# Kernel tuning notes

Measured on AMD Instinct MI355X. Metric: run time of the kernel, lower is better.

The kernel has to match this reference:

```python
import jax, jax.numpy as jnp
import numpy as np

B, S, D = 2, 4096, 512   # batch, seq_len, input_dim
W, H = 256, 4            # memory width (d_model), attention heads
DH = W // H              # per-head depth


def _dense(x, w, b):
    return x @ w + b


def setup_inputs() -> dict:
    key = jax.random.key(0)
    ks = jax.random.split(key, 24)
    def w(k, shape):
        return jax.random.normal(k, shape, dtype=jnp.float32) * 0.02
    inp = {
        "x": jax.random.normal(ks[0], (B, S, D), dtype=jnp.float32),
        # outer q/k/v projections D -> W
        "qp_w": w(ks[1], (D, W)), "qp_b": jnp.zeros((W,), jnp.float32),
        "kp_w": w(ks[2], (D, W)), "kp_b": jnp.zeros((W,), jnp.float32),
        "vp_w": w(ks[3], (D, W)), "vp_b": jnp.zeros((W,), jnp.float32),
        # MHA internal projections W -> W
        "wq_w": w(ks[4], (W, W)), "wq_b": jnp.zeros((W,), jnp.float32),
        "wk_w": w(ks[5], (W, W)), "wk_b": jnp.zeros((W,), jnp.float32),
        "wv_w": w(ks[6], (W, W)), "wv_b": jnp.zeros((W,), jnp.float32),
        "wo_w": w(ks[7], (W, W)), "wo_b": jnp.zeros((W,), jnp.float32),
        # deep MLP memory (depth=2, gelu) + its output proj W -> W
        "m0_w": w(ks[8], (W, W)), "m0_b": jnp.zeros((W,), jnp.float32),
        "m1_w": w(ks[9], (W, W)), "m1_b": jnp.zeros((W,), jnp.float32),
        "mo_w": w(ks[10], (W, W)), "mo_b": jnp.zeros((W,), jnp.float32),
        # final output projection W -> D
        "op_w": w(ks[11], (W, D)), "op_b": jnp.zeros((D,), jnp.float32),
    }
    return inp


def reference(x, qp_w, qp_b, kp_w, kp_b, vp_w, vp_b,
              wq_w, wq_b, wk_w, wk_b, wv_w, wv_b, wo_w, wo_b,
              m0_w, m0_b, m1_w, m1_b, mo_w, mo_b, op_w, op_b):
    # outer projections (D -> W)
    q0 = _dense(x, qp_w, qp_b)
    k0 = _dense(x, kp_w, kp_b)
    v0 = _dense(x, vp_w, vp_b)
    # MHA internal projections (W -> W)
    q = _dense(q0, wq_w, wq_b)
    k = _dense(k0, wk_w, wk_b)
    v = _dense(v0, wv_w, wv_b)
    # split heads: [B,S,W] -> [B,H,S,DH]
    def split(t):
        return t.reshape(B, S, H, DH).transpose(0, 2, 1, 3)
    qh, kh, vh = split(q), split(k), split(v)
    scores = jnp.einsum('bhqd,bhkd->bhqk', qh, kh) / jnp.sqrt(jnp.float32(DH))
    attn = jax.nn.softmax(scores, axis=-1)
    ctx = jnp.einsum('bhqk,bhkd->bhqd', attn, vh)
    ctx = ctx.transpose(0, 2, 1, 3).reshape(B, S, W)
    retrieved = _dense(ctx, wo_w, wo_b)
    # deep MLP memory (exact gelu, matching keras 'gelu')
    h = jax.nn.gelu(_dense(retrieved, m0_w, m0_b), approximate=False)
    h = jax.nn.gelu(_dense(h, m1_w, m1_b), approximate=False)
    mem = _dense(h, mo_w, mo_b)
    # final projection + residual
    out = _dense(mem, op_w, op_b) + x
    return out
```

## Files before the change

kernel.cpp:

```cpp
#include <hip/hip_runtime.h>
#include <cstdint>
#include <cstddef>


#define GAS(p) ((const __attribute__((address_space(1))) void*)(p))
#define LAS(p) ((__attribute__((address_space(3))) void*)(p))

typedef __attribute__((ext_vector_type(8))) short bfrag;
typedef __attribute__((ext_vector_type(4))) float facc;
typedef __attribute__((ext_vector_type(16))) float facc16;
typedef uint16_t u16;

__device__ __forceinline__ u16 f2bf(float f) {
  uint32_t u = __float_as_uint(f);
  u += 0x7fffu + ((u >> 16) & 1u);
  return (u16)(u >> 16);
}
__device__ __forceinline__ float bf2f(u16 h) {
  return __uint_as_float((uint32_t)h << 16);
}
__device__ __forceinline__ float gelu_exact(float v) {
  return 0.5f * v * (1.f + erff(v * 0.70710678118654752440f));
}
__device__ __forceinline__ facc mfma16(bfrag a, bfrag b, facc c) {
  return __builtin_amdgcn_mfma_f32_16x16x32_bf16(a, b, c, 0, 0, 0);
}
__device__ __forceinline__ facc16 mfma32(bfrag a, bfrag b, facc16 c) {
  return __builtin_amdgcn_mfma_f32_32x32x16_bf16(a, b, c, 0, 0, 0);
}

union U4 { uint32_t w[4]; bfrag f; };

__device__ __forceinline__ bfrag lds_frag(const u16* lds, int row, int kk, int ln) {
  int kb  = (kk << 6) + ((ln >> 4) << 4);
  int off = (row << 7) + (kb ^ ((row & 7) << 4));
  return *(const bfrag*)((const char*)lds + off);
}
__device__ __forceinline__ bfrag lds_frag_rb(const u16* lds, int row, int bytecol) {
  int off = (row << 7) + (bytecol ^ ((row & 7) << 4));
  return *(const bfrag*)((const char*)lds + off);
}

template <int ROWS>
__device__ __forceinline__ void stage_tile(const u16* gbase, int ldK, u16* lds,
                                           int wv, int ln) {
#pragma unroll
  for (int i = 0; i < ROWS / 32; i++) {
    int seg = (i << 2) + wv;
    int row = (seg << 3) + (ln >> 3);
    int kb  = (ln & 7) << 4;
    const char* g = (const char*)(gbase + (size_t)row * ldK) +
                    (kb ^ ((row & 7) << 4));
    __builtin_amdgcn_global_load_lds(GAS(g), LAS(lds + (seg << 9)), 16, 0, 0);
  }
}

template <int EPI, int BN>
__global__ __launch_bounds__(256) void gemm_bt(
    const u16* __restrict__ A, const u16* __restrict__ Bt,
    const float* __restrict__ bias, const float* __restrict__ resid,
    u16* __restrict__ obf, float* __restrict__ of32,
    u16* __restrict__ qb, u16* __restrict__ kb2, u16* __restrict__ vb,
    int M, int N, int K, int zsA, int zsB, int zRows) {
  const int t = threadIdx.x, wv = t >> 6, ln = t & 63;
  const int wr = wv >> 1, wc = wv & 1;
  const int m0 = blockIdx.y << 7, n0 = blockIdx.x * BN;
  const int z = blockIdx.z;
  A  += (size_t)z * zsA;
  Bt += (size_t)z * zsB;
  constexpr int NJ = BN / 32;

  __shared__ __align__(16) u16 Al[128 * 64];
  __shared__ __align__(16) u16 Bl[BN * 64];

  facc acc[4][NJ];
#pragma unroll
  for (int i = 0; i < 4; i++)
#pragma unroll
    for (int j = 0; j < NJ; j++)
#pragma unroll
      for (int r = 0; r < 4; r++) acc[i][j][r] = 0.f;

  const u16* Ab = A + (size_t)m0 * K;
  const u16* Bb = Bt + (size_t)n0 * K;
  stage_tile<128>(Ab, K, Al, wv, ln);
  stage_tile<BN>(Bb, K, Bl, wv, ln);

  const int nk = K >> 6;
  for (int kt = 0; kt < nk; ++kt) {
    __syncthreads();
#pragma unroll
    for (int kk = 0; kk < 2; kk++) {
      bfrag av[4], bv[NJ];
#pragma unroll
      for (int i = 0; i < 4; i++)
        av[i] = lds_frag(Al, (wr << 6) + (i << 4) + (ln & 15), kk, ln);
#pragma unroll
      for (int j = 0; j < NJ; j++)
        bv[j] = lds_frag(Bl, wc * (BN / 2) + (j << 4) + (ln & 15), kk, ln);
#pragma unroll
      for (int i = 0; i < 4; i++)
#pragma unroll
        for (int j = 0; j < NJ; j++)
          acc[i][j] = mfma16(av[i], bv[j], acc[i][j]);
    }
    if (kt + 1 < nk) {
      __syncthreads();
      stage_tile<128>(Ab + (kt + 1) * 64, K, Al, wv, ln);
      stage_tile<BN>(Bb + (kt + 1) * 64, K, Bl, wv, ln);
    }
  }

  const int rb = (ln >> 4) << 2, cb = ln & 15;
#pragma unroll
  for (int i = 0; i < 4; i++) {
#pragma unroll
    for (int j = 0; j < NJ; j++) {
      const int col = n0 + wc * (BN / 2) + (j << 4) + cb;
      const float bcol = bias ? bias[col] : 0.f;
#pragma unroll
      for (int r = 0; r < 4; r++) {
        const int row = m0 + (wr << 6) + (i << 4) + rb + r;
        float val = acc[i][j][r] + bcol;
        if (EPI == 0) {
          obf[(size_t)(z * zRows + row) * N + col] = f2bf(val);
        } else if (EPI == 1) {
          obf[(size_t)row * N + col] = f2bf(gelu_exact(val));
        } else if (EPI == 2) {
          const int sec = col >> 8, cc = col & 255, h = cc >> 6, dh = cc & 63;
          const int b = row >> 12, s = row & 4095;
          const size_t idx = (((size_t)(b * 4 + h)) * 4096 + s) * 64 + dh;
          if (sec == 0) qb[idx] = f2bf(val * 0.18033688011112042f);
          else if (sec == 1) kb2[idx] = f2bf(val);
          else vb[idx] = f2bf(val);
        } else {
          of32[(size_t)row * N + col] = val + resid[(size_t)row * N + col];
        }
      }
    }
  }
}

__global__ __launch_bounds__(256) void attn3(
    const u16* __restrict__ qg, const u16* __restrict__ kg,
    const u16* __restrict__ vtg, u16* __restrict__ Opart,
    float* __restrict__ lpart) {
  const int t = threadIdx.x, wv = t >> 6, ln = t & 63;
  const int l31 = ln & 31, lh = ln >> 5;
  const int qt = blockIdx.x, bh = blockIdx.y, kv = blockIdx.z;
  const int qbase = qt * 256 + wv * 64;
  const u16* Q  = qg + ((size_t)bh * 4096 + qbase) * 64;
  const u16* Kb = kg + ((size_t)bh * 4096 + kv * 1024) * 64;
  const u16* Vt = vtg + (size_t)bh * 64 * 4096 + kv * 1024;

  __shared__ __align__(16) u16 Klds[2][4096];
  __shared__ __align__(16) u16 Vlds[2][4096];

  bfrag qf[2][4];
#pragma unroll
  for (int qi = 0; qi < 2; qi++) {
    const u16* qp = Q + (size_t)(((qi << 5) + l31) << 6) + (lh << 3);
#pragma unroll
    for (int dc = 0; dc < 4; dc++)
      qf[qi][dc] = *(const bfrag*)(qp + (dc << 4));
  }
  bfrag ones;
#pragma unroll
  for (int j = 0; j < 8; j++) ones[j] = (short)0x3F80;

  facc16 oacc[2][2];
  facc16 lacc[2];
#pragma unroll
  for (int qi = 0; qi < 2; qi++) {
#pragma unroll
    for (int r = 0; r < 16; r++) {
      oacc[qi][0][r] = 0.f; oacc[qi][1][r] = 0.f; lacc[qi][r] = 0.f;
    }
  }

  stage_tile<64>(Kb, 64, Klds[0], wv, ln);
  stage_tile<64>(Vt, 4096, Vlds[0], wv, ln);

  for (int kt = 0; kt < 16; ++kt) {
    const int cur = kt & 1;
    __syncthreads();
    if (kt < 15) {
      stage_tile<64>(Kb + (size_t)(kt + 1) * 64 * 64, 64, Klds[cur ^ 1], wv, ln);
      stage_tile<64>(Vt + (kt + 1) * 64, 4096, Vlds[cur ^ 1], wv, ln);
    }
#pragma unroll
    for (int kb = 0; kb < 2; kb++) {
      bfrag kf[4];
#pragma unroll
      for (int dc = 0; dc < 4; dc++)
        kf[dc] = lds_frag_rb(Klds[cur], (kb << 5) + l31, (dc << 5) + (lh << 4));

      bfrag pa[2][2];
#pragma unroll
      for (int qi = 0; qi < 2; qi++) {
        facc16 sa;
#pragma unroll
        for (int r = 0; r < 16; r++) sa[r] = 0.f;
#pragma unroll
        for (int dc = 0; dc < 4; dc++)
          sa = mfma32(kf[dc], qf[qi][dc], sa);
        float p[16];
#pragma unroll
        for (int r = 0; r < 16; r++) p[r] = exp2f(sa[r]);
        uint32_t u0, u1, u2, u3, u4, u5, u6, u7;
        asm("v_cvt_pk_bf16_f32 %0, %1, %2" : "=v"(u0) : "v"(p[0]),  "v"(p[1]));
        asm("v_cvt_pk_bf16_f32 %0, %1, %2" : "=v"(u1) : "v"(p[2]),  "v"(p[3]));
        asm("v_cvt_pk_bf16_f32 %0, %1, %2" : "=v"(u2) : "v"(p[4]),  "v"(p[5]));
        asm("v_cvt_pk_bf16_f32 %0, %1, %2" : "=v"(u3) : "v"(p[6]),  "v"(p[7]));
        asm("v_cvt_pk_bf16_f32 %0, %1, %2" : "=v"(u4) : "v"(p[8]),  "v"(p[9]));
        asm("v_cvt_pk_bf16_f32 %0, %1, %2" : "=v"(u5) : "v"(p[10]), "v"(p[11]));
        asm("v_cvt_pk_bf16_f32 %0, %1, %2" : "=v"(u6) : "v"(p[12]), "v"(p[13]));
        asm("v_cvt_pk_bf16_f32 %0, %1, %2" : "=v"(u7) : "v"(p[14]), "v"(p[15]));
        asm volatile("v_permlane32_swap_b32 %0, %1" : "+v"(u0), "+v"(u2));
        asm volatile("v_permlane32_swap_b32 %0, %1" : "+v"(u1), "+v"(u3));
        asm volatile("v_permlane32_swap_b32 %0, %1" : "+v"(u4), "+v"(u6));
        asm volatile("v_permlane32_swap_b32 %0, %1" : "+v"(u5), "+v"(u7));
        U4 c0; c0.w[0] = u0; c0.w[1] = u1; c0.w[2] = u2; c0.w[3] = u3;
        U4 c1; c1.w[0] = u4; c1.w[1] = u5; c1.w[2] = u6; c1.w[3] = u7;
        pa[qi][0] = c0.f;
        pa[qi][1] = c1.f;
      }
#pragma unroll
      for (int c = 0; c < 2; c++) {
#pragma unroll
        for (int dj = 0; dj < 2; dj++) {
          bfrag vf = lds_frag_rb(Vlds[cur], (dj << 5) + l31,
                                 (kb << 6) + (c << 5) + (lh << 4));
          oacc[0][dj] = mfma32(pa[0][c], vf, oacc[0][dj]);
          oacc[1][dj] = mfma32(pa[1][c], vf, oacc[1][dj]);
        }
        lacc[0] = mfma32(pa[0][c], ones, lacc[0]);
        lacc[1] = mfma32(pa[1][c], ones, lacc[1]);
      }
    }
  }

  const size_t obase = (size_t)(kv * 8 + bh) * 4096 + qbase;
#pragma unroll
  for (int qi = 0; qi < 2; qi++) {
#pragma unroll
    for (int r = 0; r < 16; r++) {
      const int qrow = (qi << 5) + (r & 3) + ((r >> 2) << 3) + (lh << 2);
#pragma unroll
      for (int dj = 0; dj < 2; dj++)
        Opart[(obase + qrow) * 64 + (dj << 5) + l31] = f2bf(oacc[qi][dj][r]);
      if (l31 == 0) lpart[obase + qrow] = lacc[qi][r];
    }
  }
}

__global__ __launch_bounds__(256) void attn_combine4(
    const u16* __restrict__ Opart, const float* __restrict__ lpart,
    u16* __restrict__ ctx) {
  const int idx = blockIdx.x * 256 + threadIdx.x;
  const int d0 = (idx & 7) << 3, s = (idx >> 3) & 4095, bh = idx >> 15;
  const size_t sb = (size_t)bh * 4096 + s;
  float acc[8] = {0.f, 0.f, 0.f, 0.f, 0.f, 0.f, 0.f, 0.f};
  float lsum = 0.f;
#pragma unroll
  for (int pz = 0; pz < 4; pz++) {
    const size_t pb = (size_t)pz * 8 * 4096;
    bfrag a = *(const bfrag*)(Opart + (pb + sb) * 64 + d0);
#pragma unroll
    for (int j = 0; j < 8; j++) acc[j] += bf2f((u16)a[j]);
    lsum += lpart[pb + sb];
  }
  const float rl = 1.f / lsum;
  bfrag o;
#pragma unroll
  for (int j = 0; j < 8; j++) o[j] = (short)f2bf(acc[j] * rl);
  *(bfrag*)(ctx + ((size_t)(bh >> 2) * 4096 + s) * 256 + ((bh & 3) << 6) + d0) = o;
}

__global__ __launch_bounds__(256) void conv_all(
    const float* __restrict__ x, const float* __restrict__ qp,
    const float* __restrict__ kp, const float* __restrict__ vp,
    const float* __restrict__ mo, const float* __restrict__ wo,
    u16* __restrict__ xb, u16* __restrict__ owqkv,
    u16* __restrict__ mo_bf, u16* __restrict__ wo_bf) {
  const int bid = blockIdx.x;
  if (bid < 2048) {
    const size_t i = ((size_t)bid * 256 + threadIdx.x) * 8;
    float4 a = *(const float4*)(x + i);
    float4 b = *(const float4*)(x + i + 4);
    bfrag o;
    o[0] = (short)f2bf(a.x); o[1] = (short)f2bf(a.y);
    o[2] = (short)f2bf(a.z); o[3] = (short)f2bf(a.w);
    o[4] = (short)f2bf(b.x); o[5] = (short)f2bf(b.y);
    o[6] = (short)f2bf(b.z); o[7] = (short)f2bf(b.w);
    *(bfrag*)(xb + i) = o;
  } else {
    const int i = ((bid - 2048) * 256 + threadIdx.x) * 4;
    const float* s; u16* dst; int off;
    if (i < 131072)      { s = qp; dst = owqkv;          off = i; }
    else if (i < 262144) { s = kp; dst = owqkv + 131072; off = i - 131072; }
    else if (i < 393216) { s = vp; dst = owqkv + 262144; off = i - 262144; }
    else if (i < 458752) { s = mo; dst = mo_bf;          off = i - 393216; }
    else                 { s = wo; dst = wo_bf;          off = i - 458752; }
    float4 v = *(const float4*)(s + off);
    ushort4 o;
    o.x = f2bf(v.x); o.y = f2bf(v.y); o.z = f2bf(v.z); o.w = f2bf(v.w);
    *(ushort4*)(dst + off) = o;
  }
}

__global__ __launch_bounds__(256) void transp_all(
    const float* wq, const float* wk, const float* wv,
    const float* m0, const float* m1, const float* op_w,
    u16* wqkvT, u16* m0_t, u16* m1_t, u16* opT) {
  const int bid = blockIdx.x;
  if (bid < 1280) {
    const int mi = bid >> 8, n = bid & 255, k = threadIdx.x;
    const float* s; u16* d;
    switch (mi) {
      case 0: s = wq; d = wqkvT; break;
      case 1: s = wk; d = wqkvT + 65536; break;
      case 2: s = wv; d = wqkvT + 131072; break;
      case 3: s = m0; d = m0_t; break;
      default: s = m1; d = m1_t; break;
    }
    d[(size_t)n * 256 + k] = f2bf(s[(size_t)k * 256 + n]);
  } else {
    const int d = bid - 1280, c = threadIdx.x;
    opT[(size_t)d * 256 + c] = f2bf(op_w[(size_t)c * 512 + d]);
  }
}

__global__ __launch_bounds__(256) void fuse_bias3(
    const float* qp_b, const float* kp_b, const float* vp_b,
    const float* wq_w, const float* wk_w, const float* wv_w,
    const float* wq_b, const float* wk_b, const float* wv_b,
    const float* mo_b, const float* op_w, const float* op_b,
    const float* wo_b, const float* m0_w, const float* m0_b,
    float* bqkv, float* bmo, float* bf1) {
  const int z = blockIdx.x, t = threadIdx.x;
  __shared__ float red[4];
  float v;
  if (z < 768) {
    const int sec = z >> 8, nn = z & 255;
    const float* ob = sec == 0 ? qp_b : (sec == 1 ? kp_b : vp_b);
    const float* iw = sec == 0 ? wq_w : (sec == 1 ? wk_w : wv_w);
    v = ob[t] * iw[(size_t)t * 256 + nn];
  } else if (z < 1280) {
    v = mo_b[t] * op_w[(size_t)t * 512 + (z - 768)];
  } else {
    v = wo_b[t] * m0_w[(size_t)t * 256 + (z - 1280)];
  }
#pragma unroll
  for (int o = 32; o > 0; o >>= 1) v += __shfl_down(v, o);
  if ((t & 63) == 0) red[t >> 6] = v;
  __syncthreads();
  if (t == 0) {
    float s = red[0] + red[1] + red[2] + red[3];
    if (z < 768) {
      const int sec = z >> 8, nn = z & 255;
      const float* ib = sec == 0 ? wq_b : (sec == 1 ? wk_b : wv_b);
      bqkv[z] = s + ib[nn];
    } else if (z < 1280) {
      bmo[z - 768] = s + op_b[z - 768];
    } else {
      bf1[z - 1280] = s + m0_b[z - 1280];
    }
  }
}

__global__ __launch_bounds__(256) void transpose_v(const u16* __restrict__ v,
                                                   u16* __restrict__ vt) {
  const int bh = blockIdx.x >> 6, st = blockIdx.x & 63, t = threadIdx.x;
  __shared__ u16 tile[64][65];
  const u16* src = v + ((size_t)bh * 4096 + st * 64) * 64;
  {
    const int r = t >> 2, c0 = (t & 3) << 4;
    bfrag x0 = *(const bfrag*)(src + (size_t)r * 64 + c0);
    bfrag x1 = *(const bfrag*)(src + (size_t)r * 64 + c0 + 8);
#pragma unroll
    for (int j = 0; j < 8; j++) {
      tile[r][c0 + j] = (u16)x0[j];
      tile[r][c0 + 8 + j] = (u16)x1[j];
    }
  }
  __syncthreads();
  {
    const int d = t >> 2, s0 = (t & 3) << 4;
    bfrag y0, y1;
#pragma unroll
    for (int j = 0; j < 8; j++) {
      y0[j] = (short)tile[s0 + j][d];
      y1[j] = (short)tile[s0 + 8 + j][d];
    }
    u16* dst = vt + ((size_t)bh * 64 + d) * 4096 + (st << 6) + s0;
    *(bfrag*)(dst) = y0;
    *(bfrag*)(dst + 8) = y1;
  }
}

extern "C" void kernel_launch(void* const* d_in, const int* in_sizes, int n_in,
                              void* d_out, int out_size, void* d_ws,
                              size_t ws_size, hipStream_t stream) {
  const float* x    = (const float*)d_in[0];
  const float* qp_w = (const float*)d_in[1];
  const float* qp_b = (const float*)d_in[2];
  const float* kp_w = (const float*)d_in[3];
  const float* kp_b = (const float*)d_in[4];
  const float* vp_w = (const float*)d_in[5];
  const float* vp_b = (const float*)d_in[6];
  const float* wq_w = (const float*)d_in[7];
  const float* wq_b = (const float*)d_in[8];
  const float* wk_w = (const float*)d_in[9];
  const float* wk_b = (const float*)d_in[10];
  const float* wv_w = (const float*)d_in[11];
  const float* wv_b = (const float*)d_in[12];
  const float* wo_w = (const float*)d_in[13];
  const float* wo_b = (const float*)d_in[14];
  const float* m0_w = (const float*)d_in[15];
  const float* m0_b = (const float*)d_in[16];
  const float* m1_w = (const float*)d_in[17];
  const float* m1_b = (const float*)d_in[18];
  const float* mo_w = (const float*)d_in[19];
  const float* mo_b = (const float*)d_in[20];
  const float* op_w = (const float*)d_in[21];
  const float* op_b = (const float*)d_in[22];
  float* out = (float*)d_out;

  char* ws = (char*)d_ws;
  u16*   xb     = (u16*)(ws);
  u16*   v_buf  = (u16*)(ws + 8388608);
  u16*   Opart  = (u16*)(ws);
  u16*   q_buf  = (u16*)(ws + 16777216);
  u16*   k_buf  = (u16*)(ws + 20971520);
  u16*   vt_buf = (u16*)(ws + 25165824);
  u16*   ctx    = (u16*)(ws + 29360128);
  float* lpart  = (float*)(ws + 33554432);
  u16*   owqkv  = (u16*)(ws + 34078720);
  u16*   wqkvT  = (u16*)(ws + 34865152);
  u16*   Wqkv_t = (u16*)(ws + 35258368);
  u16*   m0_t   = (u16*)(ws + 36044800);
  u16*   m1_t   = (u16*)(ws + 36175872);
  u16*   opT    = (u16*)(ws + 36306944);
  u16*   mo_bf  = (u16*)(ws + 36569088);
  u16*   wo_bf  = (u16*)(ws + 36700160);
  u16*   Wf1_t  = (u16*)(ws + 36831232);
  u16*   Wmo_t  = (u16*)(ws + 36962304);
  float* bqkv   = (float*)(ws + 37224448);
  float* bmo    = (float*)(ws + 37227520);
  float* bf1    = (float*)(ws + 37229568);
  u16* h1 = q_buf;
  u16* h2 = k_buf;

  conv_all<<<2560, 256, 0, stream>>>(x, qp_w, kp_w, vp_w, mo_w, wo_w,
                                     xb, owqkv, mo_bf, wo_bf);
  transp_all<<<1792, 256, 0, stream>>>(wq_w, wk_w, wv_w, m0_w, m1_w, op_w,
                                       wqkvT, m0_t, m1_t, opT);
  fuse_bias3<<<1536, 256, 0, stream>>>(qp_b, kp_b, vp_b, wq_w, wk_w, wv_w,
                                       wq_b, wk_b, wv_b, mo_b, op_w, op_b,
                                       wo_b, m0_w, m0_b, bqkv, bmo, bf1);
  gemm_bt<0, 128><<<dim3(4, 2, 3), 256, 0, stream>>>(
      wqkvT, owqkv, nullptr, nullptr, Wqkv_t, nullptr, nullptr, nullptr,
      nullptr, 256, 512, 256, 65536, 131072, 256);
  gemm_bt<0, 64><<<dim3(4, 2), 256, 0, stream>>>(
      m0_t, wo_bf, nullptr, nullptr, Wf1_t, nullptr, nullptr, nullptr,
      nullptr, 256, 256, 256, 0, 0, 0);
  gemm_bt<0, 64><<<dim3(4, 4), 256, 0, stream>>>(
      opT, mo_bf, nullptr, nullptr, Wmo_t, nullptr, nullptr, nullptr,
      nullptr, 512, 256, 256, 0, 0, 0);

  gemm_bt<2, 128><<<dim3(6, 64), 256, 0, stream>>>(
      xb, Wqkv_t, bqkv, nullptr, nullptr, nullptr, q_buf, k_buf, v_buf,
      8192, 768, 512, 0, 0, 0);
  transpose_v<<<512, 256, 0, stream>>>(v_buf, vt_buf);
  attn3<<<dim3(16, 8, 4), 256, 0, stream>>>(q_buf, k_buf, vt_buf, Opart, lpart);
  attn_combine4<<<1024, 256, 0, stream>>>(Opart, lpart, ctx);

  gemm_bt<1, 64><<<dim3(4, 64), 256, 0, stream>>>(
      ctx, Wf1_t, bf1, nullptr, h1, nullptr, nullptr, nullptr, nullptr,
      8192, 256, 256, 0, 0, 0);
  gemm_bt<1, 64><<<dim3(4, 64), 256, 0, stream>>>(
      h1, m1_t, m1_b, nullptr, h2, nullptr, nullptr, nullptr, nullptr,
      8192, 256, 256, 0, 0, 0);
  gemm_bt<3, 128><<<dim3(4, 64), 256, 0, stream>>>(
      h2, Wmo_t, bmo, x, nullptr, out, nullptr, nullptr, nullptr,
      8192, 512, 256, 0, 0, 0);
}
```

Before: 271.5 us.

## Merge prep kernels, batch weight GEMMs, shrink attention blocks, add MFMA priority hints

Folds the three weight-preparation kernels (conversion, transposes, bias folding) into one prep_all launch. The transposes now go through a shared-memory tile for coalesced access, and bias folding uses per-thread loops instead of block reductions. The three small weight-composition GEMMs become a single wgemm5 launch indexed by blockIdx.z. Attention now runs with 2-wave blocks covering 128 queries each, doubling the grid. s_setprio hints are placed around the MFMA sequences in the GEMM and attention kernels. The aim is less launch overhead and better occupancy in attention, at the cost of more K/V staging traffic per query.

Result: faster. 247.7 us (-8.8%).

```diff
diff --git a/kernel.cpp b/kernel.cpp
--- a/kernel.cpp
+++ b/kernel.cpp
@@ -41,12 +41,12 @@
   return *(const bfrag*)((const char*)lds + off);
 }
 
-template <int ROWS>
+template <int ROWS, int NW>
 __device__ __forceinline__ void stage_tile(const u16* gbase, int ldK, u16* lds,
                                            int wv, int ln) {
 #pragma unroll
-  for (int i = 0; i < ROWS / 32; i++) {
-    int seg = (i << 2) + wv;
+  for (int i = 0; i < ROWS / 8 / NW; i++) {
+    int seg = i * NW + wv;
     int row = (seg << 3) + (ln >> 3);
     int kb  = (ln & 7) << 4;
     const char* g = (const char*)(gbase + (size_t)row * ldK) +
@@ -61,13 +61,10 @@
     const float* __restrict__ bias, const float* __restrict__ resid,
     u16* __restrict__ obf, float* __restrict__ of32,
     u16* __restrict__ qb, u16* __restrict__ kb2, u16* __restrict__ vb,
-    int M, int N, int K, int zsA, int zsB, int zRows) {
+    int M, int N, int K) {
   const int t = threadIdx.x, wv = t >> 6, ln = t & 63;
   const int wr = wv >> 1, wc = wv & 1;
   const int m0 = blockIdx.y << 7, n0 = blockIdx.x * BN;
-  const int z = blockIdx.z;
-  A  += (size_t)z * zsA;
-  Bt += (size_t)z * zsB;
   constexpr int NJ = BN / 32;
 
   __shared__ __align__(16) u16 Al[128 * 64];
@@ -83,8 +80,8 @@
 
   const u16* Ab = A + (size_t)m0 * K;
   const u16* Bb = Bt + (size_t)n0 * K;
-  stage_tile<128>(Ab, K, Al, wv, ln);
-  stage_tile<BN>(Bb, K, Bl, wv, ln);
+  stage_tile<128, 4>(Ab, K, Al, wv, ln);
+  stage_tile<BN, 4>(Bb, K, Bl, wv, ln);
 
   const int nk = K >> 6;
   for (int kt = 0; kt < nk; ++kt) {
@@ -98,16 +95,18 @@
 #pragma unroll
       for (int j = 0; j < NJ; j++)
         bv[j] = lds_frag(Bl, wc * (BN / 2) + (j << 4) + (ln & 15), kk, ln);
+      __builtin_amdgcn_s_setprio(1);
 #pragma unroll
       for (int i = 0; i < 4; i++)
 #pragma unroll
         for (int j = 0; j < NJ; j++)
           acc[i][j] = mfma16(av[i], bv[j], acc[i][j]);
+      __builtin_amdgcn_s_setprio(0);
     }
     if (kt + 1 < nk) {
       __syncthreads();
-      stage_tile<128>(Ab + (kt + 1) * 64, K, Al, wv, ln);
-      stage_tile<BN>(Bb + (kt + 1) * 64, K, Bl, wv, ln);
+      stage_tile<128, 4>(Ab + (kt + 1) * 64, K, Al, wv, ln);
+      stage_tile<BN, 4>(Bb + (kt + 1) * 64, K, Bl, wv, ln);
     }
   }
 
@@ -123,7 +122,7 @@
         const int row = m0 + (wr << 6) + (i << 4) + rb + r;
         float val = acc[i][j][r] + bcol;
         if (EPI == 0) {
-          obf[(size_t)(z * zRows + row) * N + col] = f2bf(val);
+          obf[(size_t)row * N + col] = f2bf(val);
         } else if (EPI == 1) {
           obf[(size_t)row * N + col] = f2bf(gelu_exact(val));
         } else if (EPI == 2) {
@@ -141,14 +140,85 @@
   }
 }
 
-__global__ __launch_bounds__(256) void attn3(
+__global__ __launch_bounds__(256) void wgemm5(
+    const u16* __restrict__ wqkvT, const u16* __restrict__ owqkv,
+    const u16* __restrict__ m0_t, const u16* __restrict__ wo_bf,
+    const u16* __restrict__ opT, const u16* __restrict__ mo_bf,
+    u16* __restrict__ Wqkv_t, u16* __restrict__ Wf1_t,
+    u16* __restrict__ Wmo_t) {
+  const int z = blockIdx.z;
+  const u16 *A, *Bt; u16* out; int M, N, rowOff;
+  if (z < 3)      { A = wqkvT + z * 65536; Bt = owqkv + z * 131072;
+                    out = Wqkv_t; M = 256; N = 512; rowOff = z * 256; }
+  else if (z == 3){ A = m0_t; Bt = wo_bf; out = Wf1_t; M = 256; N = 256; rowOff = 0; }
+  else            { A = opT;  Bt = mo_bf; out = Wmo_t; M = 512; N = 256; rowOff = 0; }
+  const int m0 = blockIdx.y << 7, n0 = blockIdx.x << 6;
+  if (m0 >= M || n0 >= N) return;
+
+  const int t = threadIdx.x, wv = t >> 6, ln = t & 63;
+  const int wr = wv >> 1, wc = wv & 1;
+  __shared__ __align__(16) u16 Al[128 * 64];
+  __shared__ __align__(16) u16 Bl[64 * 64];
+
+  facc acc[4][2];
+#pragma unroll
+  for (int i = 0; i < 4; i++)
+#pragma unroll
+    for (int j = 0; j < 2; j++)
+#pragma unroll
+      for (int r = 0; r < 4; r++) acc[i][j][r] = 0.f;
+
+  const u16* Ab = A + (size_t)m0 * 256;
+  const u16* Bb = Bt + (size_t)n0 * 256;
+  stage_tile<128, 4>(Ab, 256, Al, wv, ln);
+  stage_tile<64, 4>(Bb, 256, Bl, wv, ln);
+
+  for (int kt = 0; kt < 4; ++kt) {
+    __syncthreads();
+#pragma unroll
+    for (int kk = 0; kk < 2; kk++) {
+      bfrag av[4], bv[2];
+#pragma unroll
+      for (int i = 0; i < 4; i++)
+        av[i] = lds_frag(Al, (wr << 6) + (i << 4) + (ln & 15), kk, ln);
+#pragma unroll
+      for (int j = 0; j < 2; j++)
+        bv[j] = lds_frag(Bl, wc * 32 + (j << 4) + (ln & 15), kk, ln);
+#pragma unroll
+      for (int i = 0; i < 4; i++)
+#pragma unroll
+        for (int j = 0; j < 2; j++)
+          acc[i][j] = mfma16(av[i], bv[j], acc[i][j]);
+    }
+    if (kt + 1 < 4) {
+      __syncthreads();
+      stage_tile<128, 4>(Ab + (kt + 1) * 64, 256, Al, wv, ln);
+      stage_tile<64, 4>(Bb + (kt + 1) * 64, 256, Bl, wv, ln);
+    }
+  }
+
+  const int rb = (ln >> 4) << 2, cb = ln & 15;
+#pragma unroll
+  for (int i = 0; i < 4; i++)
+#pragma unroll
+    for (int j = 0; j < 2; j++) {
+      const int col = n0 + wc * 32 + (j << 4) + cb;
+#pragma unroll
+      for (int r = 0; r < 4; r++) {
+        const int row = m0 + (wr << 6) + (i << 4) + rb + r;
+        out[(size_t)(rowOff + row) * N + col] = f2bf(acc[i][j][r]);
+      }
+    }
+}
+
+__global__ __launch_bounds__(128) void attn4(
     const u16* __restrict__ qg, const u16* __restrict__ kg,
     const u16* __restrict__ vtg, u16* __restrict__ Opart,
     float* __restrict__ lpart) {
   const int t = threadIdx.x, wv = t >> 6, ln = t & 63;
   const int l31 = ln & 31, lh = ln >> 5;
   const int qt = blockIdx.x, bh = blockIdx.y, kv = blockIdx.z;
-  const int qbase = qt * 256 + wv * 64;
+  const int qbase = qt * 128 + wv * 64;
   const u16* Q  = qg + ((size_t)bh * 4096 + qbase) * 64;
   const u16* Kb = kg + ((size_t)bh * 4096 + kv * 1024) * 64;
   const u16* Vt = vtg + (size_t)bh * 64 * 4096 + kv * 1024;
@@ -178,15 +248,15 @@
     }
   }
 
-  stage_tile<64>(Kb, 64, Klds[0], wv, ln);
-  stage_tile<64>(Vt, 4096, Vlds[0], wv, ln);
+  stage_tile<64, 2>(Kb, 64, Klds[0], wv, ln);
+  stage_tile<64, 2>(Vt, 4096, Vlds[0], wv, ln);
 
   for (int kt = 0; kt < 16; ++kt) {
     const int cur = kt & 1;
     __syncthreads();
     if (kt < 15) {
-      stage_tile<64>(Kb + (size_t)(kt + 1) * 64 * 64, 64, Klds[cur ^ 1], wv, ln);
-      stage_tile<64>(Vt + (kt + 1) * 64, 4096, Vlds[cur ^ 1], wv, ln);
+      stage_tile<64, 2>(Kb + (size_t)(kt + 1) * 64 * 64, 64, Klds[cur ^ 1], wv, ln);
+      stage_tile<64, 2>(Vt + (kt + 1) * 64, 4096, Vlds[cur ^ 1], wv, ln);
     }
 #pragma unroll
     for (int kb = 0; kb < 2; kb++) {
@@ -201,9 +271,11 @@
         facc16 sa;
 #pragma unroll
         for (int r = 0; r < 16; r++) sa[r] = 0.f;
+        __builtin_amdgcn_s_setprio(1);
 #pragma unroll
         for (int dc = 0; dc < 4; dc++)
           sa = mfma32(kf[dc], qf[qi][dc], sa);
+        __builtin_amdgcn_s_setprio(0);
         float p[16];
 #pragma unroll
         for (int r = 0; r < 16; r++) p[r] = exp2f(sa[r]);
@@ -227,15 +299,18 @@
       }
 #pragma unroll
       for (int c = 0; c < 2; c++) {
-#pragma unroll
-        for (int dj = 0; dj < 2; dj++) {
-          bfrag vf = lds_frag_rb(Vlds[cur], (dj << 5) + l31,
-                                 (kb << 6) + (c << 5) + (lh << 4));
-          oacc[0][dj] = mfma32(pa[0][c], vf, oacc[0][dj]);
-          oacc[1][dj] = mfma32(pa[1][c], vf, oacc[1][dj]);
-        }
+        bfrag vf0 = lds_frag_rb(Vlds[cur], l31,
+                                (kb << 6) + (c << 5) + (lh << 4));
+        bfrag vf1 = lds_frag_rb(Vlds[cur], 32 + l31,
+                                (kb << 6) + (c << 5) + (lh << 4));
+        __builtin_amdgcn_s_setprio(1);
+        oacc[0][0] = mfma32(pa[0][c], vf0, oacc[0][0]);
+        oacc[1][0] = mfma32(pa[1][c], vf0, oacc[1][0]);
+        oacc[0][1] = mfma32(pa[0][c], vf1, oacc[0][1]);
+        oacc[1][1] = mfma32(pa[1][c], vf1, oacc[1][1]);
         lacc[0] = mfma32(pa[0][c], ones, lacc[0]);
         lacc[1] = mfma32(pa[1][c], ones, lacc[1]);
+        __builtin_amdgcn_s_setprio(0);
       }
     }
   }
@@ -277,15 +352,27 @@
   *(bfrag*)(ctx + ((size_t)(bh >> 2) * 4096 + s) * 256 + ((bh & 3) << 6) + d0) = o;
 }
 
-__global__ __launch_bounds__(256) void conv_all(
-    const float* __restrict__ x, const float* __restrict__ qp,
-    const float* __restrict__ kp, const float* __restrict__ vp,
-    const float* __restrict__ mo, const float* __restrict__ wo,
-    u16* __restrict__ xb, u16* __restrict__ owqkv,
-    u16* __restrict__ mo_bf, u16* __restrict__ wo_bf) {
-  const int bid = blockIdx.x;
+__global__ __launch_bounds__(256) void prep_all(
+    const float* __restrict__ x,
+    const float* __restrict__ qp, const float* __restrict__ kp,
+    const float* __restrict__ vp, const float* __restrict__ mo,
+    const float* __restrict__ wo,
+    const float* __restrict__ wq, const float* __restrict__ wk,
+    const float* __restrict__ wv, const float* __restrict__ m0,
+    const float* __restrict__ m1, const float* __restrict__ op_w,
+    const float* __restrict__ qp_b, const float* __restrict__ kp_b,
+    const float* __restrict__ vp_b, const float* __restrict__ wq_b,
+    const float* __restrict__ wk_b, const float* __restrict__ wv_b,
+    const float* __restrict__ mo_b, const float* __restrict__ op_b,
+    const float* __restrict__ wo_b, const float* __restrict__ m0_b,
+    u16* __restrict__ xb, u16* __restrict__ owqkv, u16* __restrict__ mo_bf,
+    u16* __restrict__ wo_bf, u16* __restrict__ wqkvT, u16* __restrict__ m0_t,
+    u16* __restrict__ m1_t, u16* __restrict__ opT,
+    float* __restrict__ bqkv, float* __restrict__ bmo,
+    float* __restrict__ bf1) {
+  const int bid = blockIdx.x, t = threadIdx.x;
   if (bid < 2048) {
-    const size_t i = ((size_t)bid * 256 + threadIdx.x) * 8;
+    const size_t i = ((size_t)bid * 256 + t) * 8;
     float4 a = *(const float4*)(x + i);
     float4 b = *(const float4*)(x + i + 4);
     bfrag o;
@@ -294,77 +381,87 @@
     o[4] = (short)f2bf(b.x); o[5] = (short)f2bf(b.y);
     o[6] = (short)f2bf(b.z); o[7] = (short)f2bf(b.w);
     *(bfrag*)(xb + i) = o;
-  } else {
-    const int i = ((bid - 2048) * 256 + threadIdx.x) * 4;
+  } else if (bid < 2176) {
+    const int i = (bid - 2048) * 4096 + t * 16;
     const float* s; u16* dst; int off;
     if (i < 131072)      { s = qp; dst = owqkv;          off = i; }
     else if (i < 262144) { s = kp; dst = owqkv + 131072; off = i - 131072; }
     else if (i < 393216) { s = vp; dst = owqkv + 262144; off = i - 262144; }
     else if (i < 458752) { s = mo; dst = mo_bf;          off = i - 393216; }
     else                 { s = wo; dst = wo_bf;          off = i - 458752; }
-    float4 v = *(const float4*)(s + off);
-    ushort4 o;
-    o.x = f2bf(v.x); o.y = f2bf(v.y); o.z = f2bf(v.z); o.w = f2bf(v.w);
-    *(ushort4*)(dst + off) = o;
-  }
-}
-
-__global__ __launch_bounds__(256) void transp_all(
-    const float* wq, const float* wk, const float* wv,
-    const float* m0, const float* m1, const float* op_w,
-    u16* wqkvT, u16* m0_t, u16* m1_t, u16* opT) {
-  const int bid = blockIdx.x;
-  if (bid < 1280) {
-    const int mi = bid >> 8, n = bid & 255, k = threadIdx.x;
-    const float* s; u16* d;
-    switch (mi) {
-      case 0: s = wq; d = wqkvT; break;
-      case 1: s = wk; d = wqkvT + 65536; break;
-      case 2: s = wv; d = wqkvT + 131072; break;
-      case 3: s = m0; d = m0_t; break;
-      default: s = m1; d = m1_t; break;
-    }
-    d[(size_t)n * 256 + k] = f2bf(s[(size_t)k * 256 + n]);
+    bfrag o0, o1;
+#pragma unroll
+    for (int q = 0; q < 2; q++) {
+      float4 v0 = *(const float4*)(s + off + q * 8);
+      float4 v1 = *(const float4*)(s + off + q * 8 + 4);
+      bfrag& o = q ? o1 : o0;
+      o[0] = (short)f2bf(v0.x); o[1] = (short)f2bf(v0.y);
+      o[2] = (short)f2bf(v0.z); o[3] = (short)f2bf(v0.w);
+      o[4] = (short)f2bf(v1.x); o[5] = (short)f2bf(v1.y);
+      o[6] = (short)f2bf(v1.z); o[7] = (short)f2bf(v1.w);
+    }
+    *(bfrag*)(dst + off) = o0;
+    *(bfrag*)(dst + off + 8) = o1;
+  } else if (bid < 2288) {
+    __shared__ float tile[64][65];
+    const int tid = bid - 2176;
+    const float* src; u16* dst; int r0, c0, ldS, ldD;
+    if (tid < 80) {
+      const int mi = tid >> 4, tt = tid & 15;
+      r0 = ((tt >> 2) << 6); c0 = ((tt & 3) << 6); ldS = 256; ldD = 256;
+      switch (mi) {
+        case 0: src = wq; dst = wqkvT; break;
+        case 1: src = wk; dst = wqkvT + 65536; break;
+        case 2: src = wv; dst = wqkvT + 131072; break;
+        case 3: src = m0; dst = m0_t; break;
+        default: src = m1; dst = m1_t; break;
+      }
+    } else {
+      const int tt = tid - 80;
+      r0 = ((tt >> 3) << 6); c0 = ((tt & 7) << 6);
+      ldS = 512; ldD = 256; src = op_w; dst = opT;
+    }
+    {
+      const int r = t >> 2, cc = (t & 3) << 4;
+      const float* sp = src + (size_t)(r0 + r) * ldS + c0 + cc;
+#pragma unroll
+      for (int q = 0; q < 4; q++) {
+        float4 v = *(const float4*)(sp + q * 4);
+        tile[r][cc + q * 4 + 0] = v.x; tile[r][cc + q * 4 + 1] = v.y;
+        tile[r][cc + q * 4 + 2] = v.z; tile[r][cc + q * 4 + 3] = v.w;
+      }
+    }
+    __syncthreads();
+    {
+      const int cl = t >> 2, k16 = (t & 3) << 4;
+      bfrag o0, o1;
+#pragma unroll
+      for (int j = 0; j < 8; j++) {
+        o0[j] = (short)f2bf(tile[k16 + j][cl]);
+        o1[j] = (short)f2bf(tile[k16 + 8 + j][cl]);
+      }
+      u16* dp = dst + (size_t)(c0 + cl) * ldD + r0 + k16;
+      *(bfrag*)(dp) = o0;
+      *(bfrag*)(dp + 8) = o1;
+    }
   } else {
-    const int d = bid - 1280, c = threadIdx.x;
-    opT[(size_t)d * 256 + c] = f2bf(op_w[(size_t)c * 512 + d]);
-  }
-}
-
-__global__ __launch_bounds__(256) void fuse_bias3(
-    const float* qp_b, const float* kp_b, const float* vp_b,
-    const float* wq_w, const float* wk_w, const float* wv_w,
-    const float* wq_b, const float* wk_b, const float* wv_b,
-    const float* mo_b, const float* op_w, const float* op_b,
-    const float* wo_b, const float* m0_w, const float* m0_b,
-    float* bqkv, float* bmo, float* bf1) {
-  const int z = blockIdx.x, t = threadIdx.x;
-  __shared__ float red[4];
-  float v;
-  if (z < 768) {
-    const int sec = z >> 8, nn = z & 255;
-    const float* ob = sec == 0 ? qp_b : (sec == 1 ? kp_b : vp_b);
-    const float* iw = sec == 0 ? wq_w : (sec == 1 ? wk_w : wv_w);
-    v = ob[t] * iw[(size_t)t * 256 + nn];
-  } else if (z < 1280) {
-    v = mo_b[t] * op_w[(size_t)t * 512 + (z - 768)];
-  } else {
-    v = wo_b[t] * m0_w[(size_t)t * 256 + (z - 1280)];
-  }
-#pragma unroll
-  for (int o = 32; o > 0; o >>= 1) v += __shfl_down(v, o);
-  if ((t & 63) == 0) red[t >> 6] = v;
-  __syncthreads();
-  if (t == 0) {
-    float s = red[0] + red[1] + red[2] + red[3];
-    if (z < 768) {
-      const int sec = z >> 8, nn = z & 255;
-      const float* ib = sec == 0 ? wq_b : (sec == 1 ? wk_b : wv_b);
-      bqkv[z] = s + ib[nn];
-    } else if (z < 1280) {
-      bmo[z - 768] = s + op_b[z - 768];
+    const int bz = bid - 2288;
+    if (bz < 3) {
+      const float* ob = bz == 0 ? qp_b : (bz == 1 ? kp_b : vp_b);
+      const float* iw = bz == 0 ? wq : (bz == 1 ? wk : wv);
+      const float* ib = bz == 0 ? wq_b : (bz == 1 ? wk_b : wv_b);
+      float s = 0.f;
+      for (int c = 0; c < 256; c++) s += ob[c] * iw[(size_t)c * 256 + t];
+      bqkv[bz * 256 + t] = s + ib[t];
+    } else if (bz < 5) {
+      const int d = (bz - 3) * 256 + t;
+      float s = 0.f;
+      for (int c = 0; c < 256; c++) s += mo_b[c] * op_w[(size_t)c * 512 + d];
+      bmo[d] = s + op_b[d];
     } else {
-      bf1[z - 1280] = s + m0_b[z - 1280];
+      float s = 0.f;
+      for (int c = 0; c < 256; c++) s += wo_b[c] * m0[(size_t)c * 256 + t];
+      bf1[t] = s + m0_b[t];
     }
   }
 }
@@ -452,37 +549,28 @@
   u16* h1 = q_buf;
   u16* h2 = k_buf;
 
-  conv_all<<<2560, 256, 0, stream>>>(x, qp_w, kp_w, vp_w, mo_w, wo_w,
-                                     xb, owqkv, mo_bf, wo_bf);
-  transp_all<<<1792, 256, 0, stream>>>(wq_w, wk_w, wv_w, m0_w, m1_w, op_w,
-                                       wqkvT, m0_t, m1_t, opT);
-  fuse_bias3<<<1536, 256, 0, stream>>>(qp_b, kp_b, vp_b, wq_w, wk_w, wv_w,
-                                       wq_b, wk_b, wv_b, mo_b, op_w, op_b,
-                                       wo_b, m0_w, m0_b, bqkv, bmo, bf1);
-  gemm_bt<0, 128><<<dim3(4, 2, 3), 256, 0, stream>>>(
-      wqkvT, owqkv, nullptr, nullptr, Wqkv_t, nullptr, nullptr, nullptr,
-      nullptr, 256, 512, 256, 65536, 131072, 256);
-  gemm_bt<0, 64><<<dim3(4, 2), 256, 0, stream>>>(
-      m0_t, wo_bf, nullptr, nullptr, Wf1_t, nullptr, nullptr, nullptr,
-      nullptr, 256, 256, 256, 0, 0, 0);
-  gemm_bt<0, 64><<<dim3(4, 4), 256, 0, stream>>>(
-      opT, mo_bf, nullptr, nullptr, Wmo_t, nullptr, nullptr, nullptr,
-      nullptr, 512, 256, 256, 0, 0, 0);
+  prep_all<<<2294, 256, 0, stream>>>(
+      x, qp_w, kp_w, vp_w, mo_w, wo_w,
+      wq_w, wk_w, wv_w, m0_w, m1_w, op_w,
+      qp_b, kp_b, vp_b, wq_b, wk_b, wv_b, mo_b, op_b, wo_b, m0_b,
+      xb, owqkv, mo_bf, wo_bf, wqkvT, m0_t, m1_t, opT, bqkv, bmo, bf1);
+  wgemm5<<<dim3(8, 4, 5), 256, 0, stream>>>(
+      wqkvT, owqkv, m0_t, wo_bf, opT, mo_bf, Wqkv_t, Wf1_t, Wmo_t);
 
   gemm_bt<2, 128><<<dim3(6, 64), 256, 0, stream>>>(
       xb, Wqkv_t, bqkv, nullptr, nullptr, nullptr, q_buf, k_buf, v_buf,
-      8192, 768, 512, 0, 0, 0);
+      8192, 768, 512);
   transpose_v<<<512, 256, 0, stream>>>(v_buf, vt_buf);
-  attn3<<<dim3(16, 8, 4), 256, 0, stream>>>(q_buf, k_buf, vt_buf, Opart, lpart);
+  attn4<<<dim3(32, 8, 4), 128, 0, stream>>>(q_buf, k_buf, vt_buf, Opart, lpart);
   attn_combine4<<<1024, 256, 0, stream>>>(Opart, lpart, ctx);
 
   gemm_bt<1, 64><<<dim3(4, 64), 256, 0, stream>>>(
       ctx, Wf1_t, bf1, nullptr, h1, nullptr, nullptr, nullptr, nullptr,
-      8192, 256, 256, 0, 0, 0);
+      8192, 256, 256);
   gemm_bt<1, 64><<<dim3(4, 64), 256, 0, stream>>>(
       h1, m1_t, m1_b, nullptr, h2, nullptr, nullptr, nullptr, nullptr,
-      8192, 256, 256, 0, 0, 0);
+      8192, 256, 256);
   gemm_bt<3, 128><<<dim3(4, 64), 256, 0, stream>>>(
       h2, Wmo_t, bmo, x, nullptr, out, nullptr, nullptr, nullptr,
-      8192, 512, 256, 0, 0, 0);
-}
+      8192, 512, 256);
+}
```
